# Performance work log

Hardware: AMD Instinct MI355X
Metric: run time of the kernel (lower is better)

Reference implementation:

```python
import jax, jax.numpy as jnp
import numpy as np

V, E, H, S, B = 32000, 256, 256, 128, 64
HID = 30  # DENSE_MLP_HIDDEN_SIZE


def setup_inputs() -> dict:
    key = jax.random.key(0)
    ks = jax.random.split(key, 12)
    concepts = jax.random.randint(ks[0], (S, B), 0, V)
    concepts_lengths = jax.random.randint(ks[1], (B,), 1, S + 1).at[0].set(S)
    sE = 1.0 / np.sqrt(E)
    sH = 1.0 / np.sqrt(H)
    s2H = 1.0 / np.sqrt(2 * H)
    sHID = 1.0 / np.sqrt(HID)
    return {
        "concepts": concepts,
        "concepts_lengths": concepts_lengths,
        "embedding": jax.random.normal(ks[2], (V, E), jnp.float32) * 0.02,
        "Wih_f": jax.random.normal(ks[3], (4 * H, E), jnp.float32) * sE,
        "Whh_f": jax.random.normal(ks[4], (4 * H, H), jnp.float32) * sH,
        "b_f": jax.random.normal(ks[5], (4 * H,), jnp.float32) * sH,
        "Wih_b": jax.random.normal(ks[6], (4 * H, E), jnp.float32) * sE,
        "Whh_b": jax.random.normal(ks[7], (4 * H, H), jnp.float32) * sH,
        "b_b": jax.random.normal(ks[8], (4 * H,), jnp.float32) * sH,
        "Ua": jax.random.normal(ks[9], (HID, 2 * H), jnp.float32) * s2H,
        "Wa": jax.random.normal(ks[10], (HID, 2 * H), jnp.float32) * s2H,
        "va": jax.random.normal(ks[11], (1, HID), jnp.float32) * sHID,
    }


def _lstm(x, Wih, Whh, b):
    # x: (S, B, E) -> outputs (S, B, H). PyTorch gate order: i, f, g, o.
    Bsz = x.shape[1]
    Hd = Whh.shape[1]
    h0 = jnp.zeros((Bsz, Hd), x.dtype)
    c0 = jnp.zeros((Bsz, Hd), x.dtype)

    def step(carry, xt):
        h, c = carry
        gates = xt @ Wih.T + h @ Whh.T + b
        i, f, g, o = jnp.split(gates, 4, axis=-1)
        c = jax.nn.sigmoid(f) * c + jax.nn.sigmoid(i) * jnp.tanh(g)
        h = jax.nn.sigmoid(o) * jnp.tanh(c)
        return (h, c), h

    _, hs = jax.lax.scan(step, (h0, c0), x)
    return hs


def _encode(concepts, concepts_lengths, embedding, Wih_f, Whh_f, b_f, Wih_b, Whh_b, b_b):
    emb = embedding[concepts]  # (S, B, E)
    t = jnp.arange(S)[:, None]  # (S, 1)
    lens = concepts_lengths[None, :]  # (1, B)
    valid = t < lens  # (S, B)
    # reverse each sequence within its valid length (packed biLSTM semantics)
    rev_idx = jnp.where(valid, lens - 1 - t, t)  # (S, B)
    fwd = _lstm(emb, Wih_f, Whh_f, b_f)
    x_rev = jnp.take_along_axis(emb, rev_idx[:, :, None], axis=0)
    bwd_rev = _lstm(x_rev, Wih_b, Whh_b, b_b)
    bwd = jnp.take_along_axis(bwd_rev, rev_idx[:, :, None], axis=0)
    h = jnp.concatenate([fwd, bwd], axis=-1) * valid[:, :, None]  # zero padding like pad_packed
    return h.transpose(1, 0, 2)  # (B, S, 2H)


def _edge_scores(enc, Ua, Wa, va):
    # scores[b, i, j] = va @ tanh(Ua @ enc[b,i] + Wa @ enc[b,j])
    u = enc @ Ua.T  # (B, S, HID) parent term
    w = enc @ Wa.T  # (B, S, HID) child term
    return jnp.tanh(u[:, :, None, :] + w[:, None, :, :]) @ va[0]  # (B, S, S)


def reference(concepts, concepts_lengths, embedding, Wih_f, Whh_f, b_f,
              Wih_b, Whh_b, b_b, Ua, Wa, va):
    enc = _encode(concepts, concepts_lengths, embedding,
                  Wih_f, Whh_f, b_f, Wih_b, Whh_b, b_b)
    scores = _edge_scores(enc, Ua, Wa, va)
    predictions = jnp.where(jax.nn.sigmoid(scores) >= 0.5, 1, 0)
    return scores, predictions
```

## Files before the change

kernel.cpp:

```cpp
#include <hip/hip_runtime.h>

#define V_  32000
#define E_  256
#define H_  256
#define S_  128
#define B_  64
#define HID_ 30

typedef float f32x2 __attribute__((ext_vector_type(2)));

__device__ __forceinline__ float sigmoid_acc(float x) {
    return 1.0f / (1.0f + expf(-x));
}
__device__ __forceinline__ float tanh_acc(float x) {
    return tanhf(x);
}
__device__ __forceinline__ float fast_tanh(float x) {
    return 1.f - 2.f * __builtin_amdgcn_rcpf(1.f + __expf(2.f * x));
}

__device__ __forceinline__ void store_l2x2(unsigned long long* p,
                                           unsigned long long a,
                                           unsigned long long b) {
    asm volatile("global_store_dwordx2 %2, %0, off\n\t"
                 "global_store_dwordx2 %2, %1, off offset:8"
                 :: "v"(a), "v"(b), "v"(p) : "memory");
}
__device__ __forceinline__ void load_l2x2(const unsigned long long* p,
                                          unsigned long long& a,
                                          unsigned long long& b) {
    asm volatile("global_load_dwordx2 %0, %2, off sc0\n\t"
                 "global_load_dwordx2 %1, %2, off offset:8 sc0\n\t"
                 "s_waitcnt vmcnt(0)"
                 : "=&v"(a), "=&v"(b) : "v"(p) : "memory");
}

__global__ __launch_bounds__(256) void prep_stream_kernel(
    const float* __restrict__ Whh_f, const float* __restrict__ Whh_b,
    float4* __restrict__ sT) {
    int i = blockIdx.x * 256 + threadIdx.x;
    if (i >= 12 * 1024) return;
    int r = i & 1023;
    int q = i >> 10;
    int j = q % 3;
    int side = (q % 6) / 3;
    int dir = q / 6;
    const float* Whh = dir ? Whh_b : Whh_f;
    const float* src = Whh + (size_t)r * H_ + side * 128 + 116 + 4 * j;
    sT[(size_t)q * 1024 + r] = make_float4(src[0], src[1], src[2], src[3]);
}

#define GKC 32
#define GLD 132

__global__ __launch_bounds__(256, 4) void gemm2_kernel(
    const int* __restrict__ concepts, const float* __restrict__ embedding,
    const float* __restrict__ Wih_f, const float* __restrict__ Wih_b,
    float* __restrict__ Xg) {
    __shared__ float As[GKC][GLD];
    __shared__ float Bs[GKC][GLD];
    const int dir = blockIdx.y;
    const float* Wih = dir ? Wih_b : Wih_f;
    const int mt = blockIdx.x >> 3;
    const int nt = blockIdx.x & 7;
    const int m0 = mt * 128, n0 = nt * 128;
    const int t = threadIdx.x;
    const int tm = (t & 15) * 4;
    const int tn = (t >> 4) * 4;

    int cid[4], rr[4];
#pragma unroll
    for (int i = 0; i < 4; ++i) {
        int flat = t + 256 * i;
        rr[i] = flat >> 3;
        cid[i] = concepts[m0 + rr[i]];
    }

    float acc[8][8];
#pragma unroll
    for (int i = 0; i < 8; ++i)
#pragma unroll
        for (int j = 0; j < 8; ++j) acc[i][j] = 0.f;

    for (int kk = 0; kk < E_; kk += GKC) {
        __syncthreads();
#pragma unroll
        for (int i = 0; i < 4; ++i) {
            int flat = t + 256 * i;
            int r = rr[i];
            int kq = (flat & 7) * 4;
            float4 av = *(const float4*)&embedding[(size_t)cid[i] * E_ + kk + kq];
            float4 bv = *(const float4*)&Wih[(size_t)(n0 + r) * E_ + kk + kq];
            As[kq + 0][r] = av.x; As[kq + 1][r] = av.y;
            As[kq + 2][r] = av.z; As[kq + 3][r] = av.w;
            Bs[kq + 0][r] = bv.x; Bs[kq + 1][r] = bv.y;
            Bs[kq + 2][r] = bv.z; Bs[kq + 3][r] = bv.w;
        }
        __syncthreads();
#pragma unroll
        for (int k = 0; k < GKC; ++k) {
            float4 a0 = *(const float4*)&As[k][tm];
            float4 a1 = *(const float4*)&As[k][tm + 64];
            float4 b0 = *(const float4*)&Bs[k][tn];
            float4 b1 = *(const float4*)&Bs[k][tn + 64];
            float am[8] = {a0.x, a0.y, a0.z, a0.w, a1.x, a1.y, a1.z, a1.w};
            float bn[8] = {b0.x, b0.y, b0.z, b0.w, b1.x, b1.y, b1.z, b1.w};
#pragma unroll
            for (int i = 0; i < 8; ++i)
#pragma unroll
                for (int j = 0; j < 8; ++j)
                    acc[i][j] = fmaf(am[i], bn[j], acc[i][j]);
        }
    }
    float* out = Xg + ((size_t)dir * 8192 + m0) * 1024 + n0;
#pragma unroll
    for (int i = 0; i < 8; ++i) {
        int mr = (i < 4) ? (tm + i) : (tm + 60 + i);
        *(float4*)&out[(size_t)mr * 1024 + tn] =
            make_float4(acc[i][0], acc[i][1], acc[i][2], acc[i][3]);
        *(float4*)&out[(size_t)mr * 1024 + tn + 64] =
            make_float4(acc[i][4], acc[i][5], acc[i][6], acc[i][7]);
    }
}

#define RP_ 39
#define LP_ 19

__global__ __launch_bounds__(512, 2) void lstm_ks3_kernel(
    const float* __restrict__ Xg,
    const float* __restrict__ Whh_f, const float* __restrict__ Whh_b,
    const float* __restrict__ b_f, const float* __restrict__ b_b,
    const int* __restrict__ lens,
    float* __restrict__ enc,
    unsigned long long* __restrict__ Fch,
    unsigned long long* __restrict__ Sch,
    const float4* __restrict__ sT) {
    extern __shared__ f32x2 Wl[];
    __shared__ f32x2 h_sh2[64];
    __shared__ float g_sh[2][128];
    const int w = blockIdx.x;
    const int side = w >> 7;
    const int P = w & 127;
    const int dir = P & 1, b = P >> 1;
    const int t = threadIdx.x;
    const int r0 = t, r1 = t + 512;
    const int ul = t & 127;
    const int gc = t >> 8;
    const bool mine = (((t >> 7) & 1) == side);
    const int base = side << 7;
    const int idx = (gc << 7) + ul;
    const float* Whh = dir ? Whh_b : Whh_f;
    const int len = lens[b];

    f32x2 w0[RP_], w1[RP_];
    {
        const f32x2* p0 = (const f32x2*)(Whh + (size_t)r0 * H_ + base);
        const f32x2* p1 = (const f32x2*)(Whh + (size_t)r1 * H_ + base);
#pragma unroll
        for (int j = 0; j < RP_; ++j) { w0[j] = p0[j]; w1[j] = p1[j]; }
#pragma unroll
        for (int j = 0; j < LP_; ++j) {
            Wl[j * 1024 + r0] = p0[RP_ + j];
            Wl[j * 1024 + r1] = p1[RP_ + j];
        }
    }
    const float* bias = dir ? b_b : b_f;
    const float bias0 = bias[r0], bias1 = bias[r1];
    const float4* sT0 = sT + (size_t)(dir * 6 + side * 3) * 1024;

    unsigned long long* fw0 = Fch + (((size_t)P * 2 + 0) * 2 + side) * 512 + 2 * idx;
    unsigned long long* fw1 = Fch + (((size_t)P * 2 + 1) * 2 + side) * 512 + 2 * idx;
    const unsigned long long* fr0 =
        Fch + (((size_t)P * 2 + 0) * 2 + (side ^ 1)) * 512 + 2 * idx;
    const unsigned long long* fr1 =
        Fch + (((size_t)P * 2 + 1) * 2 + (side ^ 1)) * 512 + 2 * idx;
    unsigned long long* sw0 = Sch + (((size_t)P * 2 + 0) * 2 + side) * 512 + 2 * idx;
    unsigned long long* sw1 = Sch + (((size_t)P * 2 + 1) * 2 + side) * 512 + 2 * idx;
    const unsigned long long* sr0 =
        Sch + (((size_t)P * 2 + 0) * 2 + (side ^ 1)) * 512 + 2 * idx;
    const unsigned long long* sr1 =
        Sch + (((size_t)P * 2 + 1) * 2 + (side ^ 1)) * 512 + 2 * idx;

    if (t < 64) h_sh2[t] = (f32x2){0.f, 0.f};
    float c = 0.f;
    __syncthreads();

    int srow = dir ? (len - 1) : 0;
    float x0 = 0.f, x1 = 0.f;
    if (mine) {
        const float* xp = Xg + ((size_t)dir * 8192 + (size_t)srow * B_ + b) * 1024;
        x0 = xp[r0]; x1 = xp[r1];
    }

    for (int s = 0; s < S_; ++s) {
        float4 s00 = sT0[r0], s01 = sT0[1024 + r0], s02 = sT0[2048 + r0];
        float4 s10 = sT0[r1], s11 = sT0[1024 + r1], s12 = sT0[2048 + r1];
        int srow_n = 0;
        float x0n = 0.f, x1n = 0.f;
        if (s + 1 < S_) {
            int ns = s + 1;
            srow_n = dir ? ((ns < len) ? (len - 1 - ns) : ns) : ns;
            if (mine) {
                const float* xp =
                    Xg + ((size_t)dir * 8192 + (size_t)srow_n * B_ + b) * 1024;
                x0n = xp[r0]; x1n = xp[r1];
            }
        }

        f32x2 a0 = (f32x2){0.f, 0.f}, a1 = (f32x2){0.f, 0.f};
#pragma unroll
        for (int j = 0; j < RP_; ++j) {
            f32x2 hv = h_sh2[j];
            a0 = __builtin_elementwise_fma(w0[j], hv, a0);
            a1 = __builtin_elementwise_fma(w1[j], hv, a1);
        }
#pragma unroll
        for (int j = 0; j < LP_; ++j) {
            f32x2 hv = h_sh2[RP_ + j];
            f32x2 wa = Wl[j * 1024 + r0];
            f32x2 wb = Wl[j * 1024 + r1];
            a0 = __builtin_elementwise_fma(wa, hv, a0);
            a1 = __builtin_elementwise_fma(wb, hv, a1);
        }
        {
            f32x2 h58 = h_sh2[58], h59 = h_sh2[59], h60 = h_sh2[60];
            f32x2 h61 = h_sh2[61], h62 = h_sh2[62], h63 = h_sh2[63];
            a0 = __builtin_elementwise_fma((f32x2){s00.x, s00.y}, h58, a0);
            a0 = __builtin_elementwise_fma((f32x2){s00.z, s00.w}, h59, a0);
            a0 = __builtin_elementwise_fma((f32x2){s01.x, s01.y}, h60, a0);
            a0 = __builtin_elementwise_fma((f32x2){s01.z, s01.w}, h61, a0);
            a0 = __builtin_elementwise_fma((f32x2){s02.x, s02.y}, h62, a0);
            a0 = __builtin_elementwise_fma((f32x2){s02.z, s02.w}, h63, a0);
            a1 = __builtin_elementwise_fma((f32x2){s10.x, s10.y}, h58, a1);
            a1 = __builtin_elementwise_fma((f32x2){s10.z, s10.w}, h59, a1);
            a1 = __builtin_elementwise_fma((f32x2){s11.x, s11.y}, h60, a1);
            a1 = __builtin_elementwise_fma((f32x2){s11.z, s11.w}, h61, a1);
            a1 = __builtin_elementwise_fma((f32x2){s12.x, s12.y}, h62, a1);
            a1 = __builtin_elementwise_fma((f32x2){s12.z, s12.w}, h63, a1);
        }
        float p0 = a0.x + a0.y, p1 = a1.x + a1.y;

        const unsigned tag = (unsigned)(s + 1);
        float iv = 0.f, gv = 0.f;
        if (!mine) {
            unsigned long long k0 =
                ((unsigned long long)tag << 32) | (unsigned long long)__float_as_uint(p0);
            unsigned long long k1 =
                ((unsigned long long)tag << 32) | (unsigned long long)__float_as_uint(p1);
            store_l2x2((s & 1) ? fw1 : fw0, k0, k1);
            unsigned long long* sb = (s & 1) ? sw1 : sw0;
            __hip_atomic_store(sb, k0, __ATOMIC_RELAXED, __HIP_MEMORY_SCOPE_AGENT);
            __hip_atomic_store(sb + 1, k1, __ATOMIC_RELAXED, __HIP_MEMORY_SCOPE_AGENT);
        } else {
            const unsigned long long* fr = (s & 1) ? fr1 : fr0;
            const unsigned long long* sr = (s & 1) ? sr1 : sr0;
            float q0f, q1f;
            for (;;) {
                unsigned long long f0, f1;
                load_l2x2(fr, f0, f1);
                if ((unsigned)(f0 >> 32) == tag && (unsigned)(f1 >> 32) == tag) {
                    q0f = __uint_as_float((unsigned)f0);
                    q1f = __uint_as_float((unsigned)f1);
                    break;
                }
                unsigned long long a0q = __hip_atomic_load(
                    sr, __ATOMIC_RELAXED, __HIP_MEMORY_SCOPE_AGENT);
                unsigned long long a1q = __hip_atomic_load(
                    sr + 1, __ATOMIC_RELAXED, __HIP_MEMORY_SCOPE_AGENT);
                if ((unsigned)(a0q >> 32) == tag && (unsigned)(a1q >> 32) == tag) {
                    q0f = __uint_as_float((unsigned)a0q);
                    q1f = __uint_as_float((unsigned)a1q);
                    break;
                }
            }
            float g0 = p0 + q0f + bias0 + x0;
            float g1 = p1 + q1f + bias1 + x1;
            if (gc == 0) {
                iv = sigmoid_acc(g0);
                gv = tanh_acc(g1);
            } else {
                g_sh[0][ul] = sigmoid_acc(g0);
                g_sh[1][ul] = sigmoid_acc(g1);
            }
        }
        __syncthreads();

        if (mine && gc == 0) {
            float fv = g_sh[0][ul], ov = g_sh[1][ul];
            c = fv * c + iv * gv;
            float h = ov * tanh_acc(c);
            ((float*)h_sh2)[ul] = h;
            int orow = dir ? srow : s;
            enc[((size_t)b * S_ + orow) * 512 + dir * H_ + base + ul] =
                (orow < len) ? h : 0.f;
        }
        __syncthreads();

        srow = srow_n;
        x0 = x0n; x1 = x1n;
    }
}

__global__ __launch_bounds__(256) void uw_kernel(
    const float* __restrict__ enc, const float* __restrict__ Ua,
    const float* __restrict__ Wa, float* __restrict__ U, float* __restrict__ Wout) {
    __shared__ float wgt[60][129];
    __shared__ float erow[4][128];
    const int tid = threadIdx.x;
    const int b = blockIdx.y, s0 = blockIdx.x * 32;
    const int rl = tid >> 6;
    const int d = tid & 63;
    const int dd = d & 31;
    const int isW = d >> 5;
    float acc[8];
#pragma unroll
    for (int i = 0; i < 8; ++i) acc[i] = 0.f;

    for (int kk = 0; kk < 4; ++kk) {
        __syncthreads();
        for (int i = tid; i < 30 * 128; i += 256) {
            int r = i >> 7, k = i & 127;
            wgt[r][k] = Ua[(size_t)r * 512 + kk * 128 + k];
            wgt[r + 30][k] = Wa[(size_t)r * 512 + kk * 128 + k];
        }
        for (int chunk = 0; chunk < 8; ++chunk) {
            __syncthreads();
            for (int i = tid; i < 4 * 128; i += 256) {
                int r = i >> 7, k = i & 127;
                erow[r][k] = enc[((size_t)b * S_ + (s0 + chunk * 4 + r)) * 512 + kk * 128 + k];
            }
            __syncthreads();
            if (dd < HID_) {
                const float* wr = wgt[dd + 30 * isW];
                const float* er = erow[rl];
                float a = acc[chunk];
#pragma unroll
                for (int k = 0; k < 128; ++k) a = fmaf(er[k], wr[k], a);
                acc[chunk] = a;
            }
        }
    }
    if (dd < HID_) {
        float* dst = isW ? Wout : U;
#pragma unroll
        for (int chunk = 0; chunk < 8; ++chunk)
            dst[((size_t)b * S_ + (s0 + chunk * 4 + rl)) * 32 + dd] = acc[chunk];
    }
}

__global__ __launch_bounds__(256) void scores_kernel(
    const float* __restrict__ U, const float* __restrict__ W,
    const float* __restrict__ va,
    float* __restrict__ scores, float* __restrict__ preds) {
    __shared__ float w_sh[128][31];
    const int b = blockIdx.y, i0 = blockIdx.x * 32;
    const int tid = threadIdx.x;

    float va_r[HID_];
#pragma unroll
    for (int d2 = 0; d2 < HID_; ++d2) va_r[d2] = va[d2];

    for (int i = tid; i < 128 * HID_; i += 256) {
        int r = i / HID_, d2 = i - r * HID_;
        w_sh[r][d2] = W[((size_t)b * S_ + r) * 32 + d2];
    }
    __syncthreads();

    const int il = tid >> 3;
    const int jb = (tid & 7) * 16;
    float u_r[HID_];
    const float* urow = U + ((size_t)b * S_ + i0 + il) * 32;
#pragma unroll
    for (int d2 = 0; d2 < HID_; ++d2) u_r[d2] = urow[d2];

    const size_t obase = ((size_t)b * S_ + (i0 + il)) * S_;
    for (int jj = 0; jj < 16; ++jj) {
        int j = jb + jj;
        float acc = 0.f;
#pragma unroll
        for (int d2 = 0; d2 < HID_; ++d2)
            acc = fmaf(va_r[d2], fast_tanh(u_r[d2] + w_sh[j][d2]), acc);
        scores[obase + j] = acc;
        preds[obase + j] = (sigmoid_acc(acc) >= 0.5f) ? 1.f : 0.f;
    }
}

extern "C" void kernel_launch(void* const* d_in, const int* in_sizes, int n_in,
                              void* d_out, int out_size, void* d_ws, size_t ws_size,
                              hipStream_t stream) {
    (void)in_sizes; (void)n_in; (void)out_size; (void)ws_size;
    const int* concepts = (const int*)d_in[0];
    const int* lens = (const int*)d_in[1];
    const float* embedding = (const float*)d_in[2];
    const float* Wih_f = (const float*)d_in[3];
    const float* Whh_f = (const float*)d_in[4];
    const float* b_f = (const float*)d_in[5];
    const float* Wih_b = (const float*)d_in[6];
    const float* Whh_b = (const float*)d_in[7];
    const float* b_b = (const float*)d_in[8];
    const float* Ua = (const float*)d_in[9];
    const float* Wa = (const float*)d_in[10];
    const float* va = (const float*)d_in[11];

    char* ws = (char*)d_ws;
    float* Xg = (float*)(ws + 0);
    float* enc = (float*)(ws + 67108864);
    float* U = (float*)(ws + 83886080);
    float* W = (float*)(ws + 84934656);
    unsigned long long* Fch = (unsigned long long*)(ws + 85983232);
    unsigned long long* Sch = (unsigned long long*)(ws + 88080384);
    float4* sT = (float4*)(ws + 90177536);

    float* scores = (float*)d_out;
    float* preds = scores + (size_t)B_ * S_ * S_;

    (void)hipMemsetAsync(Fch, 0, 2 * 2097152, stream);

    hipLaunchKernelGGL(prep_stream_kernel, dim3(48), dim3(256), 0, stream,
                       Whh_f, Whh_b, sT);
    hipLaunchKernelGGL(gemm2_kernel, dim3(512, 2), dim3(256), 0, stream,
                       concepts, embedding, Wih_f, Wih_b, Xg);

    {
        const float* XgA = Xg;
        void* ka[] = {(void*)&XgA, (void*)&Whh_f, (void*)&Whh_b, (void*)&b_f,
                      (void*)&b_b, (void*)&lens, (void*)&enc, (void*)&Fch,
                      (void*)&Sch, (void*)&sT};
        (void)hipLaunchCooperativeKernel((const void*)lstm_ks3_kernel, dim3(256),
                                         dim3(512), ka, LP_ * 1024 * sizeof(f32x2),
                                         stream);
    }

    hipLaunchKernelGGL(uw_kernel, dim3(4, 64), dim3(256), 0, stream,
                       enc, Ua, Wa, U, W);
    hipLaunchKernelGGL(scores_kernel, dim3(4, 64), dim3(256), 0, stream,
                       U, W, va, scores, preds);
}
```

Measured before the change: 598.6 us.

## Pair LSTM chain blocks on the same XCD via runtime registration

Each LSTM block reads its hardware XCC id, registers itself in a global table, and waits at a grid-wide barrier until all blocks have registered. The two blocks (sides) of each recurrent chain are then assigned from blocks on the same XCD, falling back to cross-XCD pairs for leftovers. The goal is to keep the per-step partner exchange inside one XCD's L2 instead of crossing dies. The cost is an extra startup barrier, a serial table scan by one thread per block, and a memset.

```diff
diff --git a/kernel.cpp b/kernel.cpp
--- a/kernel.cpp
+++ b/kernel.cpp
@@ -8,6 +8,8 @@
 #define HID_ 30
 
 typedef float f32x2 __attribute__((ext_vector_type(2)));
+
+#define HWREG_XCC_ID ((3 << 11) | 20)
 
 __device__ __forceinline__ float sigmoid_acc(float x) {
     return 1.0f / (1.0f + expf(-x));
@@ -126,7 +128,7 @@
 #define RP_ 39
 #define LP_ 19
 
-__global__ __launch_bounds__(512, 2) void lstm_ks3_kernel(
+__global__ __launch_bounds__(512, 2) void lstm_ks4_kernel(
     const float* __restrict__ Xg,
     const float* __restrict__ Whh_f, const float* __restrict__ Whh_b,
     const float* __restrict__ b_f, const float* __restrict__ b_b,
@@ -134,15 +136,65 @@
     float* __restrict__ enc,
     unsigned long long* __restrict__ Fch,
     unsigned long long* __restrict__ Sch,
-    const float4* __restrict__ sT) {
+    const float4* __restrict__ sT,
+    int* __restrict__ Reg) {
     extern __shared__ f32x2 Wl[];
     __shared__ f32x2 h_sh2[64];
     __shared__ float g_sh[2][128];
+    __shared__ int s_tab[8 + 512];
+    __shared__ int s_info[2];
     const int w = blockIdx.x;
-    const int side = w >> 7;
-    const int P = w & 127;
+    const int t = threadIdx.x;
+
+    if (t == 0) {
+        int xcd = __builtin_amdgcn_s_getreg(HWREG_XCC_ID) & 7;
+        int slot = __hip_atomic_fetch_add(&Reg[xcd], 1, __ATOMIC_RELAXED,
+                                          __HIP_MEMORY_SCOPE_AGENT) & 63;
+        __hip_atomic_store(&Reg[16 + xcd * 64 + slot], w + 1, __ATOMIC_RELAXED,
+                           __HIP_MEMORY_SCOPE_AGENT);
+        __hip_atomic_fetch_add(&Reg[8], 1, __ATOMIC_RELEASE,
+                               __HIP_MEMORY_SCOPE_AGENT);
+        while (__hip_atomic_load(&Reg[8], __ATOMIC_ACQUIRE,
+                                 __HIP_MEMORY_SCOPE_AGENT) < 256)
+            __builtin_amdgcn_s_sleep(2);
+    }
+    __syncthreads();
+    if (t < 8)
+        s_tab[t] = __hip_atomic_load(&Reg[t], __ATOMIC_RELAXED,
+                                     __HIP_MEMORY_SCOPE_AGENT);
+    if (t < 512)
+        s_tab[8 + t] = __hip_atomic_load(&Reg[16 + t], __ATOMIC_RELAXED,
+                                         __HIP_MEMORY_SCOPE_AGENT);
+    __syncthreads();
+    if (t == 0) {
+        int chain = 0, side = 0, pc = 0;
+        int lef[8];
+        int nl = 0;
+        for (int x = 0; x < 8; ++x) {
+            int c = s_tab[x];
+            if (c > 64) c = 64;
+            for (int i = 0; i + 1 < c; i += 2) {
+                int wa = s_tab[8 + x * 64 + i] - 1;
+                int wb = s_tab[8 + x * 64 + i + 1] - 1;
+                if (wa == w) { chain = pc; side = 0; }
+                if (wb == w) { chain = pc; side = 1; }
+                ++pc;
+            }
+            if (c & 1) lef[nl++] = s_tab[8 + x * 64 + c - 1] - 1;
+        }
+        for (int i = 0; i + 1 < nl; i += 2) {
+            if (lef[i] == w)     { chain = pc; side = 0; }
+            if (lef[i + 1] == w) { chain = pc; side = 1; }
+            ++pc;
+        }
+        s_info[0] = chain;
+        s_info[1] = side;
+    }
+    __syncthreads();
+    const int P = s_info[0];
+    const int side = s_info[1];
     const int dir = P & 1, b = P >> 1;
-    const int t = threadIdx.x;
+
     const int r0 = t, r1 = t + 512;
     const int ul = t & 127;
     const int gc = t >> 8;
@@ -410,11 +462,13 @@
     unsigned long long* Fch = (unsigned long long*)(ws + 85983232);
     unsigned long long* Sch = (unsigned long long*)(ws + 88080384);
     float4* sT = (float4*)(ws + 90177536);
+    int* Reg = (int*)(ws + 90374144);
 
     float* scores = (float*)d_out;
     float* preds = scores + (size_t)B_ * S_ * S_;
 
     (void)hipMemsetAsync(Fch, 0, 2 * 2097152, stream);
+    (void)hipMemsetAsync(Reg, 0, 4096, stream);
 
     hipLaunchKernelGGL(prep_stream_kernel, dim3(48), dim3(256), 0, stream,
                        Whh_f, Whh_b, sT);
@@ -425,8 +479,8 @@
         const float* XgA = Xg;
         void* ka[] = {(void*)&XgA, (void*)&Whh_f, (void*)&Whh_b, (void*)&b_f,
                       (void*)&b_b, (void*)&lens, (void*)&enc, (void*)&Fch,
-                      (void*)&Sch, (void*)&sT};
-        (void)hipLaunchCooperativeKernel((const void*)lstm_ks3_kernel, dim3(256),
+                      (void*)&Sch, (void*)&sT, (void*)&Reg};
+        (void)hipLaunchCooperativeKernel((const void*)lstm_ks4_kernel, dim3(256),
                                          dim3(512), ka, LP_ * 1024 * sizeof(f32x2),
                                          stream);
     }
```

Result: no change. 604.3 us (+1.0%).
